# Kernel tuning notes

Measured on AMD Instinct MI355X. Metric: run time of the kernel, lower is better.

## Reference

```python
import jax, jax.numpy as jnp
import numpy as np

N_EMBD = 1024
HEAD_SIZE = 128
B, T = 8, 2048


def apply_rope(x):
    # x: (B, T, D); rotate interleaved pairs, matching torch view(B,T,D//2,2)
    b, t, d = x.shape
    freqs = 1.0 / (10000.0 ** (jnp.arange(0, d, 2, dtype=jnp.float32) / d))  # (D//2,)
    angles = jnp.arange(t, dtype=jnp.float32)[:, None] * freqs[None, :]      # (T, D//2)
    cos_a = jnp.cos(angles).astype(x.dtype)
    sin_a = jnp.sin(angles).astype(x.dtype)
    xr = x.reshape(b, t, d // 2, 2)
    x0, x1 = xr[..., 0], xr[..., 1]
    rot = jnp.stack([x0 * cos_a - x1 * sin_a, x0 * sin_a + x1 * cos_a], axis=-1)
    return rot.reshape(b, t, d)


def setup_inputs() -> dict:
    key = jax.random.key(0)
    kx, kq, kk, kv = jax.random.split(key, 4)
    x = jax.random.normal(kx, (B, T, N_EMBD), dtype=jnp.float32)
    scale = 0.02
    Wq = jax.random.normal(kq, (N_EMBD, HEAD_SIZE), dtype=jnp.float32) * scale
    Wk = jax.random.normal(kk, (N_EMBD, HEAD_SIZE), dtype=jnp.float32) * scale
    Wv = jax.random.normal(kv, (N_EMBD, HEAD_SIZE), dtype=jnp.float32) * scale
    return {"x": x, "Wq": Wq, "Wk": Wk, "Wv": Wv}


def reference(x, Wq, Wk, Wv):
    # QKV projections (bias=False)
    q = x @ Wq  # (B, T, H)
    k = x @ Wk
    v = x @ Wv
    q = apply_rope(q)
    k = apply_rope(k)
    d = k.shape[-1]
    wei = jnp.einsum('bqd,bkd->bqk', q, k) * (d ** -0.5)  # (B, T, T)
    causal = jnp.tril(jnp.ones((q.shape[1], q.shape[1]), dtype=bool))
    wei = jnp.where(causal, wei, jnp.finfo(wei.dtype).min)
    wei = jax.nn.softmax(wei, axis=-1)
    out = jnp.einsum('bqk,bkd->bqd', wei, v)  # (B, T, H)
    return out
```

## Files before the change

### kernel.cpp

```cpp
#include <hip/hip_runtime.h>
#include <math.h>

#define BB 8
#define TT 2048
#define EE 1024
#define DD 128

typedef _Float16 f16x8 __attribute__((ext_vector_type(8)));
typedef _Float16 f16x4 __attribute__((ext_vector_type(4)));
typedef float    f32x4 __attribute__((ext_vector_type(4)));
typedef float    f32x16 __attribute__((ext_vector_type(16)));

#define QSCALE 0.12752406f


__global__ __launch_bounds__(256)
void wt_prep_kernel(const float* __restrict__ Wq,
                    const float* __restrict__ Wk,
                    const float* __restrict__ Wv,
                    _Float16* __restrict__ Wb)
{
    int gid = blockIdx.x * 256 + threadIdx.x;
    int kc  = gid / 768;
    int rem = gid - kc * 768;
    int ns  = rem >> 6;
    int ln  = rem & 63;
    int n   = ns * 32 + (ln & 31);
    int k0  = kc * 16 + (ln >> 5) * 8;
    const float* __restrict__ W = (n < 128) ? Wq : (n < 256) ? Wk : Wv;
    int nl = n & 127;
    f16x8 w;
#pragma unroll
    for (int j = 0; j < 8; j++)
        w[j] = (_Float16)W[(size_t)(k0 + j) * DD + nl];
    *(f16x8*)&Wb[(size_t)gid * 8] = w;
}

__global__ __launch_bounds__(256)
void proj_rope_kernel(const float* __restrict__ x,
                      const _Float16* __restrict__ Wb,
                      _Float16* __restrict__ Qb,
                      _Float16* __restrict__ Ka,
                      _Float16* __restrict__ Va)
{
    const int r0   = blockIdx.x * 32;
    const int tid  = threadIdx.x;
    const int wave = tid >> 6;
    const int lane = tid & 63;
    const int half = lane >> 5;
    const int col  = lane & 31;

    __shared__ _Float16 Xb[2][2048];
    __shared__ _Float16 Out[32][136];

    f32x16 acc[3];
#pragma unroll
    for (int s = 0; s < 3; s++) acc[s] = (f32x16)0.f;

    const int sr = tid >> 3;
    const int sc = (tid & 7) * 4;
    const float* __restrict__ xp = &x[(size_t)(r0 + sr) * EE + sc];
    const int w0 = ((sc        >> 4) << 9) + ((sr + 32 * ((sc        >> 3) & 1)) << 3) + (sc & 7);
    const int w1 = (((sc + 32) >> 4) << 9) + ((sr + 32 * (((sc + 32) >> 3) & 1)) << 3) + (sc & 7);

    float4 pa0 = *(const float4*)(xp);
    float4 pa1 = *(const float4*)(xp + 32);
    {
        f16x4 h0 = { (_Float16)pa0.x, (_Float16)pa0.y, (_Float16)pa0.z, (_Float16)pa0.w };
        f16x4 h1 = { (_Float16)pa1.x, (_Float16)pa1.y, (_Float16)pa1.z, (_Float16)pa1.w };
        *(f16x4*)&Xb[0][w0] = h0;
        *(f16x4*)&Xb[0][w1] = h1;
    }
    float4 na0 = *(const float4*)(xp + 64);
    float4 na1 = *(const float4*)(xp + 96);
    float4 nb0 = *(const float4*)(xp + 128);
    float4 nb1 = *(const float4*)(xp + 160);

    for (int it = 0; it < 16; it++) {
        const int buf = it & 1;
        __syncthreads();
        f16x8 a[4], b[12];
#pragma unroll
        for (int kc = 0; kc < 4; kc++)
            a[kc] = *(f16x8*)&Xb[buf][(kc << 9) + lane * 8];
#pragma unroll
        for (int kc = 0; kc < 4; kc++)
#pragma unroll
            for (int s = 0; s < 3; s++)
                b[kc * 3 + s] = *(const f16x8*)&Wb[((size_t)(it * 4 + kc) * 12 + wave * 3 + s) * 512 + lane * 8];
#pragma unroll
        for (int kc = 0; kc < 4; kc++)
#pragma unroll
            for (int s = 0; s < 3; s++)
                acc[s] = __builtin_amdgcn_mfma_f32_32x32x16_f16(a[kc], b[kc * 3 + s], acc[s], 0, 0, 0);
        if (it + 1 < 16) {
            f16x4 h0 = { (_Float16)na0.x, (_Float16)na0.y, (_Float16)na0.z, (_Float16)na0.w };
            f16x4 h1 = { (_Float16)na1.x, (_Float16)na1.y, (_Float16)na1.z, (_Float16)na1.w };
            *(f16x4*)&Xb[buf ^ 1][w0] = h0;
            *(f16x4*)&Xb[buf ^ 1][w1] = h1;
            na0 = nb0; na1 = nb1;
        }
        if (it + 3 < 16) {
            nb0 = *(const float4*)(xp + (it + 3) * 64);
            nb1 = *(const float4*)(xp + (it + 3) * 64 + 32);
        }
    }

    const int bidx = r0 >> 11;
    const int t0   = r0 & (TT - 1);

    for (int p = 0; p < 3; p++) {
        __syncthreads();
#pragma unroll
        for (int s = 0; s < 3; s++) {
            int gs = wave * 3 + s;
            if ((gs >> 2) != p) continue;
            int dcol = (gs & 3) * 32 + col;
            float f = 0.f;
            if (p < 2)
                f = __powf(10000.0f, -(float)(dcol & ~1) * (1.0f / 128.0f));
#pragma unroll
            for (int rg = 0; rg < 16; rg++) {
                int mrow = (rg & 3) + 8 * (rg >> 2) + 4 * half;
                float av = acc[s][rg];
                float res;
                if (p < 2) {
                    float ap = __shfl_xor(av, 1);
                    float sa, ca;
                    __sincosf((float)(t0 + mrow) * f, &sa, &ca);
                    res = av * ca + ap * ((dcol & 1) ? sa : -sa);
                    if (p == 0) res *= QSCALE;
                } else {
                    res = av;
                }
                Out[mrow][dcol] = (_Float16)res;
            }
        }
        __syncthreads();
        if (p < 2) {
            _Float16* __restrict__ dst = (p == 0) ? Qb : Ka;
#pragma unroll
            for (int jj = 0; jj < 2; jj++) {
                int cid = tid + 256 * jj;
                int kc = cid >> 6, ln = cid & 63;
                f16x8 v8 = *(f16x8*)&Out[ln & 31][kc * 16 + (ln >> 5) * 8];
                size_t ga = ((((size_t)bidx * 64 + (t0 >> 5)) * 8 + kc) * 64 + ln) * 8;
                *(f16x8*)&dst[ga] = v8;
            }
        } else {
#pragma unroll
            for (int jj = 0; jj < 2; jj++) {
                int cid = tid + 256 * jj;
                int kcl = cid >> 8, ds = (cid >> 6) & 3, ln = cid & 63;
                f16x8 vv;
#pragma unroll
                for (int e = 0; e < 8; e++)
                    vv[e] = Out[kcl * 16 + (ln >> 5) * 8 + e][ds * 32 + (ln & 31)];
                size_t ga = ((((size_t)bidx * 128 + (t0 >> 4) + kcl) * 4 + ds) * 64 + ln) * 8;
                *(f16x8*)&Va[ga] = vv;
            }
        }
    }
}

__global__ __launch_bounds__(256)
void attn_kernel(const _Float16* __restrict__ Qb,
                 const _Float16* __restrict__ Ka,
                 const _Float16* __restrict__ Va,
                 _Float16* __restrict__ opart,
                 float* __restrict__ mpart,
                 float* __restrict__ lpart)
{
    const int b = blockIdx.y;
    int xt = 15, c = 0;
    {
        int v = 71 - blockIdx.x, s0 = 0;
        for (int j = 0; j < 16; j++) {
            int nc = (j + 2) >> 1;
            if (v < s0 + nc) { xt = j; c = v - s0; break; }
            s0 += nc;
        }
    }
    const int q0 = xt * 128;
    const int nt = 2 * xt + 2;
    const int kt_begin = c * 4;
    const int kt_end   = (kt_begin + 4 < nt) ? (kt_begin + 4) : nt;

    const int tid  = threadIdx.x;
    const int wave = tid >> 6;
    const int lane = tid & 63;
    const int half = lane >> 5;
    const int col  = lane & 31;

    __shared__ _Float16 Kb[8192];
    __shared__ _Float16 Vb[8192];
    __shared__ _Float16 Ps[4][32][72];

    const _Float16* __restrict__ kst = Ka + (size_t)b * 64 * 4096;
    const _Float16* __restrict__ vst = Va + (size_t)b * 128 * 2048;

    const int qg = q0 + wave * 32 + col;
    f16x8 qb[8];
#pragma unroll
    for (int kc = 0; kc < 8; kc++)
        qb[kc] = *(const f16x8*)&Qb[((((size_t)b * 64 + xt * 4 + wave) * 8 + kc) * 64 + lane) * 8];

    f32x16 Of[4];
#pragma unroll
    for (int t = 0; t < 4; t++) Of[t] = (f32x16)0.f;
    float m_ = -1e30f, l_ = 0.f;

    f16x8 kr[4], vr[4];
    {
        const _Float16* kp = kst + (size_t)kt_begin * 8192;
        const _Float16* vp = vst + (size_t)kt_begin * 8192;
#pragma unroll
        for (int i = 0; i < 4; i++) kr[i] = *(const f16x8*)&kp[(tid + 256 * i) * 8];
#pragma unroll
        for (int i = 0; i < 4; i++) vr[i] = *(const f16x8*)&vp[(tid + 256 * i) * 8];
    }

    for (int kt = kt_begin; kt < kt_end; kt++) {
        const int kb0 = kt * 64;
        __syncthreads();
#pragma unroll
        for (int i = 0; i < 4; i++) *(f16x8*)&Kb[(tid + 256 * i) * 8] = kr[i];
#pragma unroll
        for (int i = 0; i < 4; i++) *(f16x8*)&Vb[(tid + 256 * i) * 8] = vr[i];
        __syncthreads();
        if (kt + 1 < kt_end) {
            const _Float16* kp = kst + (size_t)(kt + 1) * 8192;
            const _Float16* vp = vst + (size_t)(kt + 1) * 8192;
#pragma unroll
            for (int i = 0; i < 4; i++) kr[i] = *(const f16x8*)&kp[(tid + 256 * i) * 8];
#pragma unroll
            for (int i = 0; i < 4; i++) vr[i] = *(const f16x8*)&vp[(tid + 256 * i) * 8];
        }

        f32x16 sf[2];
#pragma unroll
        for (int g = 0; g < 2; g++) {
            sf[g] = (f32x16)0.f;
#pragma unroll
            for (int kc = 0; kc < 8; kc++) {
                f16x8 kf = *(f16x8*)&Kb[((g * 8 + kc) * 64 + lane) * 8];
                sf[g] = __builtin_amdgcn_mfma_f32_32x32x16_f16(kf, qb[kc], sf[g], 0, 0, 0);
            }
        }

        const bool diag = (kt >= 2 * xt);
        float mloc = -1e30f;
#pragma unroll
        for (int g = 0; g < 2; g++)
#pragma unroll
            for (int rg = 0; rg < 16; rg++) {
                int key = kb0 + g * 32 + (rg & 3) + 8 * (rg >> 2) + 4 * half;
                float val = sf[g][rg];
                val = (!diag || key <= qg) ? val : -1e30f;
                sf[g][rg] = val;
                mloc = fmaxf(mloc, val);
            }
        mloc = fmaxf(mloc, __shfl_xor(mloc, 32));
        float mnew  = fmaxf(m_, mloc);
        float alpha = __builtin_amdgcn_exp2f(m_ - mnew);
        float ps = 0.f;
#pragma unroll
        for (int g = 0; g < 2; g++) {
#pragma unroll
            for (int rc = 0; rc < 4; rc++) {
                f16x4 p4;
#pragma unroll
                for (int rr = 0; rr < 4; rr++) {
                    float p = __builtin_amdgcn_exp2f(sf[g][4 * rc + rr] - mnew);
                    ps += p;
                    p4[rr] = (_Float16)p;
                }
                *(f16x4*)&Ps[wave][col][g * 32 + 8 * rc + 4 * half] = p4;
            }
        }
        ps += __shfl_xor(ps, 32);
        l_ = l_ * alpha + ps;
        m_ = mnew;
#pragma unroll
        for (int t = 0; t < 4; t++) Of[t] *= alpha;

        f16x8 pb[4];
#pragma unroll
        for (int kc = 0; kc < 4; kc++)
            pb[kc] = *(f16x8*)&Ps[wave][col][kc * 16 + half * 8];
#pragma unroll
        for (int t = 0; t < 4; t++) {
#pragma unroll
            for (int kcl = 0; kcl < 4; kcl++) {
                f16x8 vf = *(f16x8*)&Vb[((kcl * 4 + t) * 64 + lane) * 8];
                Of[t] = __builtin_amdgcn_mfma_f32_32x32x16_f16(vf, pb[kcl], Of[t], 0, 0, 0);
            }
        }
    }

    const int slot = (b * 16 + xt) * 8 + c;
    _Float16* op = opart + ((size_t)slot * 128 + wave * 32 + col) * DD;
#pragma unroll
    for (int t = 0; t < 4; t++) {
#pragma unroll
        for (int rc = 0; rc < 4; rc++) {
            f16x4 o4 = { (_Float16)Of[t][4 * rc + 0], (_Float16)Of[t][4 * rc + 1],
                         (_Float16)Of[t][4 * rc + 2], (_Float16)Of[t][4 * rc + 3] };
            *(f16x4*)&op[t * 32 + 8 * rc + 4 * half] = o4;
        }
    }
    if (half == 0) {
        mpart[slot * 128 + wave * 32 + col] = m_;
        lpart[slot * 128 + wave * 32 + col] = l_;
    }
}

__global__ __launch_bounds__(256)
void combine_kernel(const _Float16* __restrict__ opart,
                    const float* __restrict__ mpart,
                    const float* __restrict__ lpart,
                    float* __restrict__ out)
{
    int gid = blockIdx.x * 256 + threadIdx.x;
    int d   = gid & 127;
    int t   = gid >> 7;
    int b   = t >> 11;
    int tl  = t & (TT - 1);
    int xt  = tl >> 7;
    int rl  = tl & 127;
    int np  = (2 * xt + 5) >> 2;
    int sb  = (b * 16 + xt) * 8;

    float mm = -1e30f;
    for (int j = 0; j < np; j++)
        mm = fmaxf(mm, mpart[(sb + j) * 128 + rl]);
    float acc = 0.f, den = 0.f;
    for (int j = 0; j < np; j++) {
        float w = __builtin_amdgcn_exp2f(mpart[(sb + j) * 128 + rl] - mm);
        den += w * lpart[(sb + j) * 128 + rl];
        acc += w * (float)opart[((size_t)(sb + j) * 128 + rl) * DD + d];
    }
    out[gid] = acc / den;
}

extern "C" void kernel_launch(void* const* d_in, const int* in_sizes, int n_in,
                              void* d_out, int out_size, void* d_ws, size_t ws_size,
                              hipStream_t stream)
{
    const float* x  = (const float*)d_in[0];
    const float* Wq = (const float*)d_in[1];
    const float* Wk = (const float*)d_in[2];
    const float* Wv = (const float*)d_in[3];
    float* out = (float*)d_out;

    const size_t NTOK = (size_t)BB * TT;
    _Float16* Qb = (_Float16*)d_ws;
    _Float16* Ka = Qb + NTOK * DD;
    _Float16* Va = Ka + NTOK * DD;
    _Float16* Wb = Va + NTOK * DD;
    _Float16* opart = Wb + (size_t)384 * EE;
    float* mp = (float*)(opart + (size_t)1024 * 128 * DD);
    float* lp = mp + 1024 * 128;

    wt_prep_kernel<<<dim3(192), dim3(256), 0, stream>>>(Wq, Wk, Wv, Wb);
    proj_rope_kernel<<<dim3(512), dim3(256), 0, stream>>>(x, Wb, Qb, Ka, Va);
    attn_kernel<<<dim3(72, BB), dim3(256), 0, stream>>>(Qb, Ka, Va, opart, mp, lp);
    combine_kernel<<<dim3((int)(NTOK * DD / 256)), dim3(256), 0, stream>>>(opart, mp, lp, out);
}
```

Before: 170.5 us.

## Split attention into finer two-tile KV chunks and relax barriers and occupancy hints

The attention split-KV decomposition changes from chunks of up to four 64-key tiles (72 blocks per batch) to fixed two-tile chunks (136 blocks per batch). Block order is no longer reversed and the partial-result buffers and combine indexing grow to match. The goal is better load balance and more parallelism, at the cost of more partial writes and more combine reads. Barriers become a raw lgkmcnt wait plus s_barrier, launch bounds request two blocks per CU, and the next x prefetch in the projection is issued before the MFMAs.

```diff
diff --git a/kernel.cpp b/kernel.cpp
--- a/kernel.cpp
+++ b/kernel.cpp
@@ -12,6 +12,8 @@
 typedef float    f32x16 __attribute__((ext_vector_type(16)));
 
 #define QSCALE 0.12752406f
+
+#define BAR_LGKM() asm volatile("s_waitcnt lgkmcnt(0)\n\ts_barrier" ::: "memory")
 
 
 __global__ __launch_bounds__(256)
@@ -36,7 +38,7 @@
     *(f16x8*)&Wb[(size_t)gid * 8] = w;
 }
 
-__global__ __launch_bounds__(256)
+__global__ __launch_bounds__(256, 2)
 void proj_rope_kernel(const float* __restrict__ x,
                       const _Float16* __restrict__ Wb,
                       _Float16* __restrict__ Qb,
@@ -78,7 +80,7 @@
 
     for (int it = 0; it < 16; it++) {
         const int buf = it & 1;
-        __syncthreads();
+        BAR_LGKM();
         f16x8 a[4], b[12];
 #pragma unroll
         for (int kc = 0; kc < 4; kc++)
@@ -88,6 +90,12 @@
 #pragma unroll
             for (int s = 0; s < 3; s++)
                 b[kc * 3 + s] = *(const f16x8*)&Wb[((size_t)(it * 4 + kc) * 12 + wave * 3 + s) * 512 + lane * 8];
+        float4 nc0, nc1;
+        const bool have_nc = (it + 3 < 16);
+        if (have_nc) {
+            nc0 = *(const float4*)(xp + (it + 3) * 64);
+            nc1 = *(const float4*)(xp + (it + 3) * 64 + 32);
+        }
 #pragma unroll
         for (int kc = 0; kc < 4; kc++)
 #pragma unroll
@@ -99,10 +107,7 @@
             *(f16x4*)&Xb[buf ^ 1][w0] = h0;
             *(f16x4*)&Xb[buf ^ 1][w1] = h1;
             na0 = nb0; na1 = nb1;
-        }
-        if (it + 3 < 16) {
-            nb0 = *(const float4*)(xp + (it + 3) * 64);
-            nb1 = *(const float4*)(xp + (it + 3) * 64 + 32);
+            if (have_nc) { nb0 = nc0; nb1 = nc1; }
         }
     }
 
@@ -110,7 +115,7 @@
     const int t0   = r0 & (TT - 1);
 
     for (int p = 0; p < 3; p++) {
-        __syncthreads();
+        BAR_LGKM();
 #pragma unroll
         for (int s = 0; s < 3; s++) {
             int gs = wave * 3 + s;
@@ -136,7 +141,7 @@
                 Out[mrow][dcol] = (_Float16)res;
             }
         }
-        __syncthreads();
+        BAR_LGKM();
         if (p < 2) {
             _Float16* __restrict__ dst = (p == 0) ? Qb : Ka;
 #pragma unroll
@@ -163,7 +168,7 @@
     }
 }
 
-__global__ __launch_bounds__(256)
+__global__ __launch_bounds__(256, 2)
 void attn_kernel(const _Float16* __restrict__ Qb,
                  const _Float16* __restrict__ Ka,
                  const _Float16* __restrict__ Va,
@@ -174,17 +179,14 @@
     const int b = blockIdx.y;
     int xt = 15, c = 0;
     {
-        int v = 71 - blockIdx.x, s0 = 0;
+        int v = blockIdx.x, s0 = 0;
         for (int j = 0; j < 16; j++) {
-            int nc = (j + 2) >> 1;
-            if (v < s0 + nc) { xt = j; c = v - s0; break; }
-            s0 += nc;
-        }
-    }
-    const int q0 = xt * 128;
-    const int nt = 2 * xt + 2;
-    const int kt_begin = c * 4;
-    const int kt_end   = (kt_begin + 4 < nt) ? (kt_begin + 4) : nt;
+            if (v < s0 + j + 1) { xt = j; c = v - s0; break; }
+            s0 += j + 1;
+        }
+    }
+    const int q0  = xt * 128;
+    const int kt0 = 2 * c;
 
     const int tid  = threadIdx.x;
     const int wave = tid >> 6;
@@ -199,6 +201,16 @@
     const _Float16* __restrict__ kst = Ka + (size_t)b * 64 * 4096;
     const _Float16* __restrict__ vst = Va + (size_t)b * 128 * 2048;
 
+    f16x8 kr[4], vr[4];
+    {
+        const _Float16* kp = kst + (size_t)kt0 * 8192;
+        const _Float16* vp = vst + (size_t)kt0 * 8192;
+#pragma unroll
+        for (int i = 0; i < 4; i++) kr[i] = *(const f16x8*)&kp[(tid + 256 * i) * 8];
+#pragma unroll
+        for (int i = 0; i < 4; i++) vr[i] = *(const f16x8*)&vp[(tid + 256 * i) * 8];
+    }
+
     const int qg = q0 + wave * 32 + col;
     f16x8 qb[8];
 #pragma unroll
@@ -210,27 +222,19 @@
     for (int t = 0; t < 4; t++) Of[t] = (f32x16)0.f;
     float m_ = -1e30f, l_ = 0.f;
 
-    f16x8 kr[4], vr[4];
-    {
-        const _Float16* kp = kst + (size_t)kt_begin * 8192;
-        const _Float16* vp = vst + (size_t)kt_begin * 8192;
-#pragma unroll
-        for (int i = 0; i < 4; i++) kr[i] = *(const f16x8*)&kp[(tid + 256 * i) * 8];
-#pragma unroll
-        for (int i = 0; i < 4; i++) vr[i] = *(const f16x8*)&vp[(tid + 256 * i) * 8];
-    }
-
-    for (int kt = kt_begin; kt < kt_end; kt++) {
+#pragma unroll
+    for (int tt = 0; tt < 2; tt++) {
+        const int kt  = kt0 + tt;
         const int kb0 = kt * 64;
-        __syncthreads();
+        BAR_LGKM();
 #pragma unroll
         for (int i = 0; i < 4; i++) *(f16x8*)&Kb[(tid + 256 * i) * 8] = kr[i];
 #pragma unroll
         for (int i = 0; i < 4; i++) *(f16x8*)&Vb[(tid + 256 * i) * 8] = vr[i];
-        __syncthreads();
-        if (kt + 1 < kt_end) {
-            const _Float16* kp = kst + (size_t)(kt + 1) * 8192;
-            const _Float16* vp = vst + (size_t)(kt + 1) * 8192;
+        BAR_LGKM();
+        if (tt == 0) {
+            const _Float16* kp = kst + (size_t)(kt0 + 1) * 8192;
+            const _Float16* vp = vst + (size_t)(kt0 + 1) * 8192;
 #pragma unroll
             for (int i = 0; i < 4; i++) kr[i] = *(const f16x8*)&kp[(tid + 256 * i) * 8];
 #pragma unroll
@@ -298,7 +302,7 @@
         }
     }
 
-    const int slot = (b * 16 + xt) * 8 + c;
+    const int slot = (b * 16 + xt) * 16 + c;
     _Float16* op = opart + ((size_t)slot * 128 + wave * 32 + col) * DD;
 #pragma unroll
     for (int t = 0; t < 4; t++) {
@@ -328,8 +332,8 @@
     int tl  = t & (TT - 1);
     int xt  = tl >> 7;
     int rl  = tl & 127;
-    int np  = (2 * xt + 5) >> 2;
-    int sb  = (b * 16 + xt) * 8;
+    int np  = xt + 1;
+    int sb  = (b * 16 + xt) * 16;
 
     float mm = -1e30f;
     for (int j = 0; j < np; j++)
@@ -359,11 +363,11 @@
     _Float16* Va = Ka + NTOK * DD;
     _Float16* Wb = Va + NTOK * DD;
     _Float16* opart = Wb + (size_t)384 * EE;
-    float* mp = (float*)(opart + (size_t)1024 * 128 * DD);
-    float* lp = mp + 1024 * 128;
+    float* mp = (float*)(opart + (size_t)2048 * 128 * DD);
+    float* lp = mp + 2048 * 128;
 
     wt_prep_kernel<<<dim3(192), dim3(256), 0, stream>>>(Wq, Wk, Wv, Wb);
     proj_rope_kernel<<<dim3(512), dim3(256), 0, stream>>>(x, Wb, Qb, Ka, Va);
-    attn_kernel<<<dim3(72, BB), dim3(256), 0, stream>>>(Qb, Ka, Va, opart, mp, lp);
+    attn_kernel<<<dim3(136, BB), dim3(256), 0, stream>>>(Qb, Ka, Va, opart, mp, lp);
     combine_kernel<<<dim3((int)(NTOK * DD / 256)), dim3(256), 0, stream>>>(opart, mp, lp, out);
 }
```

Measured after the change: 188.6 us. 10.6% more time.
